# Kernel optimization log

Measured on AMD Instinct MI355X. Metric: run time of the kernel, lower is better.

The kernel has to match this reference:

```python
import jax, jax.numpy as jnp
import numpy as np

KER = 8

def _gelu(x):
    return jax.nn.gelu(x, approximate=False)

def _conv3x3(x, w, b):
    y = jax.lax.conv_general_dilated(x, w, (1, 1), 'SAME',
                                     dimension_numbers=('NCHW', 'OIHW', 'NCHW'))
    return y + b[None, :, None, None]

def _unfold(x):
    # F.unfold(kernel=8, stride=8): [B,C,H,W] -> [B, C*64, L], C-major then kh,kw
    B, C, H, W = x.shape
    Hb, Wb = H // KER, W // KER
    p = x.reshape(B, C, Hb, KER, Wb, KER).transpose(0, 1, 3, 5, 2, 4)
    return p.reshape(B, C * KER * KER, Hb * Wb)

def _fold(cols, H, W):
    # inverse of _unfold (non-overlapping patches)
    B, CK, L = cols.shape
    C = CK // (KER * KER)
    Hb, Wb = H // KER, W // KER
    p = cols.reshape(B, C, KER, KER, Hb, Wb).transpose(0, 1, 4, 2, 5, 3)
    return p.reshape(B, C, H, W)

def _bn(x, g, b, eps=1e-5):
    # train-mode BatchNorm1d on [B, C, L]: stats over (B, L) per channel
    m = x.mean(axis=(0, 2), keepdims=True)
    v = x.var(axis=(0, 2), keepdims=True)
    return (x - m) * jax.lax.rsqrt(v + eps) * g[None, :, None] + b[None, :, None]


def setup_inputs() -> dict:
    key = jax.random.key(0)
    ks = jax.random.split(key, 10)
    ind, d, hid = 64, 1024, 256
    f = lambda k, s: jax.random.normal(k, s, dtype=jnp.float32) * 0.02
    return {
        'feat': jax.random.normal(ks[0], (4, ind, 256, 256), dtype=jnp.float32),
        'w_enc': f(ks[1], (ind, ind, 3, 3)), 'b_enc': jnp.zeros((ind,), jnp.float32),
        'w_k': f(ks[2], (ind, ind, 3, 3)), 'b_k': jnp.zeros((ind,), jnp.float32),
        'w_v': f(ks[3], (ind, ind, 3, 3)), 'b_v': jnp.zeros((ind,), jnp.float32),
        'fcq_w': f(ks[4], (d, ind * KER * KER)), 'fcq_b': jnp.zeros((d,), jnp.float32),
        'fck_w': f(ks[5], (d, ind * KER * KER)), 'fck_b': jnp.zeros((d,), jnp.float32),
        'bnq_g': jnp.ones((d,), jnp.float32), 'bnq_b': jnp.zeros((d,), jnp.float32),
        'bnk_g': jnp.ones((d,), jnp.float32), 'bnk_b': jnp.zeros((d,), jnp.float32),
        'ff1_w': f(ks[6], (hid, ind)), 'ff1_b': jnp.zeros((hid,), jnp.float32),
        'ff2_w': f(ks[7], (ind, hid)), 'ff2_b': jnp.zeros((ind,), jnp.float32),
    }


def reference(feat, w_enc, b_enc, w_k, b_k, w_v, b_v,
              fcq_w, fcq_b, fck_w, fck_b, bnq_g, bnq_b, bnk_g, bnk_b,
              ff1_w, ff1_b, ff2_w, ff2_b):
    B, C, H, W = feat.shape
    fk = _gelu(_conv3x3(feat, w_k, b_k))
    fv = _gelu(_conv3x3(feat, w_v, b_v))
    refer = _gelu(_conv3x3(feat, w_enc, b_enc))
    q_un = _unfold(refer).transpose(0, 2, 1)   # [B, L, C*64]
    k_un = _unfold(fk).transpose(0, 2, 1)
    v_un = _unfold(fv).transpose(0, 2, 1)
    q = jnp.einsum('blc,dc->bld', q_un, fcq_w) + fcq_b
    q = _bn(q.transpose(0, 2, 1), bnq_g, bnq_b).transpose(0, 2, 1)  # [B, L, 1024]
    k = jnp.einsum('blc,dc->bld', k_un, fck_w) + fck_b
    k = _bn(k.transpose(0, 2, 1), bnk_g, bnk_b).transpose(0, 2, 1)
    scores = jnp.einsum('bld,bmd->blm', q, k) / jnp.sqrt(jnp.float32(q.shape[2]))
    attn = jax.nn.softmax(scores, axis=2)
    out = jnp.einsum('blm,bmc->blc', attn, v_un).transpose(0, 2, 1)  # [B, C*64, L]
    out = _fold(out, H, W)
    h = _gelu(jnp.einsum('bchw,oc->bohw', out, ff1_w) + ff1_b[None, :, None, None])
    h = _gelu(jnp.einsum('bchw,oc->bohw', h, ff2_w) + ff2_b[None, :, None, None])
    return h + feat
```

## Files before the change

kernel.cpp:

```cpp
#include <hip/hip_runtime.h>

typedef unsigned short u16;
typedef float f4 __attribute__((ext_vector_type(4)));
typedef float f32x4 __attribute__((ext_vector_type(4)));
typedef short bf16x8 __attribute__((ext_vector_type(8)));
typedef u16 u16x8 __attribute__((ext_vector_type(8)));
typedef u16 u16x4 __attribute__((ext_vector_type(4)));

__device__ __forceinline__ u16 f2bf(float f){
  unsigned u = __float_as_uint(f);
  u = (u + 0x7FFFu + ((u>>16)&1u)) >> 16;
  return (u16)u;
}
__device__ __forceinline__ float bf2f(u16 u){
  return __uint_as_float(((unsigned)u)<<16);
}
__device__ __forceinline__ float gelu_f(float x){
  float y = 1.5957691216057308f*(x + 0.044715f*x*x*x);
  y = fminf(y, 30.0f);
  float t = __expf(y);
  float r = __builtin_amdgcn_rcpf(t + 1.0f);
  return 0.5f*x*(1.0f + (t - 1.0f)*r);
}

typedef __attribute__((address_space(1))) const unsigned int as1_cuint;
typedef __attribute__((address_space(3))) unsigned int as3_uint;
__device__ __forceinline__ void gload_lds16(const void* g, void* l){
  __builtin_amdgcn_global_load_lds((as1_cuint*)g, (as3_uint*)l, 16, 0, 0);
}

__global__ __launch_bounds__(256) void to_nhwc(
    const float* __restrict__ F, u16* __restrict__ O)
{
  __shared__ float tile[64][65];
  const int t = threadIdx.x, b = blockIdx.y;
  const long px0 = (long)blockIdx.x*64;
  const float* Fb = F + (long)b*64*65536;
  #pragma unroll
  for (int i = 0; i < 4; ++i){
    const int ch = (t>>4) + i*16;
    const int pxo = (t&15)*4;
    f4 v = *(const f4*)&Fb[(long)ch*65536 + px0 + pxo];
    tile[ch][pxo]=v[0]; tile[ch][pxo+1]=v[1]; tile[ch][pxo+2]=v[2]; tile[ch][pxo+3]=v[3];
  }
  __syncthreads();
  const int px = t & 63, ch0 = (t>>6)*16;
  u16x8 o0, o1;
  #pragma unroll
  for (int j = 0; j < 8; ++j){ o0[j]=f2bf(tile[ch0+j][px]); o1[j]=f2bf(tile[ch0+8+j][px]); }
  u16* Ob = O + ((long)b*65536 + px0 + px)*64 + ch0;
  *(u16x8*)Ob = o0; *(u16x8*)(Ob+8) = o1;
}

__global__ __launch_bounds__(256) void wt_prep(
    const float* __restrict__ we, const float* __restrict__ wk,
    const float* __restrict__ wv, u16* __restrict__ Wt2)
{
  const int i = blockIdx.x*256 + threadIdx.x;
  const int cio = i & 31;
  const int t1 = i >> 5;
  const int n  = t1 % 192;
  const int t2 = t1 / 192;
  const int kc = t2 & 1, p = t2 >> 1;
  const int dy = p/3, dx = p - dy*3;
  const int ci = kc*32 + cio;
  const float* W = (n < 64) ? we : (n < 128) ? wk : wv;
  const int co = n & 63;
  Wt2[i] = f2bf(W[((co*64 + ci)*3 + dy)*3 + dx]);
}

__global__ __launch_bounds__(512,2) void conv_mfma(
    const u16* __restrict__ X, const u16* __restrict__ Wt2,
    const float* __restrict__ be, const float* __restrict__ bk, const float* __restrict__ bv,
    u16* __restrict__ Aq, u16* __restrict__ Ak, u16* __restrict__ Vl)
{
  __shared__ __align__(16) u16 smem[24576];
  const int t = threadIdx.x, lane = t & 63, wvi = t >> 6;
  const int bx = blockIdx.x, by = blockIdx.y, b = blockIdx.z;
  const int x0 = bx*16, y0 = by*8;
  const u16* Xb = X + (long)b*4194304;

  #pragma unroll
  for (int j = 0; j < 3; ++j){
    const int id = t + j*512;
    if (id < 1440){
      const int row = id / 144, rem = id - row*144, col = rem >> 3, ck = rem & 7;
      const int y = y0 - 1 + row, x = x0 - 1 + col;
      int4 v = {0,0,0,0};
      if ((unsigned)y < 256u && (unsigned)x < 256u)
        v = *(const int4*)(Xb + ((long)y*256 + x)*64 + ck*8);
      *(int4*)&smem[((row*18 + col)*8 + (ck ^ (col&7)))*8] = v;
    }
  }
  __syncthreads();

  const int wm4 = (wvi>>2)*4;
  const int wn  = (wvi&3)*48;
  const int fr = lane & 15, fo = lane >> 4;
  f32x4 acc[4][3] = {};

  #pragma unroll
  for (int dy = 0; dy < 3; ++dy)
  #pragma unroll
  for (int dx = 0; dx < 3; ++dx){
    const int p = dy*3 + dx;
    #pragma unroll
    for (int kc = 0; kc < 2; ++kc){
      bf16x8 af[4], bfv[3];
      const u16* wp = Wt2 + ((long)(p*2 + kc)*192 + wn + fr)*32 + fo*8;
      #pragma unroll
      for (int ni = 0; ni < 3; ++ni)
        bfv[ni] = *(const bf16x8*)(wp + ni*16*32);
      #pragma unroll
      for (int mi = 0; mi < 4; ++mi){
        const int row = wm4 + mi + dy;
        const int col = fr + dx;
        af[mi] = *(const bf16x8*)&smem[((row*18 + col)*8 + ((kc*4+fo) ^ (col&7)))*8];
      }
      #pragma unroll
      for (int mi = 0; mi < 4; ++mi)
        #pragma unroll
        for (int ni = 0; ni < 3; ++ni)
          acc[mi][ni] = __builtin_amdgcn_mfma_f32_16x16x32_bf16(af[mi], bfv[ni], acc[mi][ni], 0, 0, 0);
    }
  }
  __syncthreads();

  const int c0 = fo*4;
  const int lloc = c0 >> 3, kw0 = c0 & 7;
  #pragma unroll
  for (int ni = 0; ni < 3; ++ni){
    const int n = wn + ni*16 + fr;
    const int mat = n >> 6, co = n & 63;
    const float bias = (mat==0) ? be[co] : (mat==1) ? bk[co] : bv[co];
    #pragma unroll
    for (int mi = 0; mi < 4; ++mi){
      const int r = wm4 + mi;
      u16x4 o;
      #pragma unroll
      for (int rg = 0; rg < 4; ++rg) o[rg] = f2bf(gelu_f(acc[mi][ni][rg] + bias));
      const int e = ((mat*2 + lloc)*64 + co)*64 + ((r*8 + kw0) ^ ((co&7)<<3));
      *(u16x4*)&smem[e] = o;
    }
  }
  __syncthreads();

  const int l_lo = by*32 + bx*2;
  const int co_r = t >> 3, sw = (t&7) ^ (co_r&7);
  const int eoff = co_r*64 + sw*8;
  #pragma unroll
  for (int i = 0; i < 6; ++i){
    const int mat = i >> 1, ll = i & 1;
    u16x8 v = *(const u16x8*)&smem[(mat*2 + ll)*4096 + eoff];
    u16* dst = (mat==0 ? Aq : mat==1 ? Ak : Vl)
             + ((long)b*1024 + l_lo + ll)*4096 + t*8;
    *(u16x8*)dst = v;
  }
}

__global__ __launch_bounds__(256) void v_tr(
    const u16* __restrict__ S, u16* __restrict__ D)
{
  __shared__ u16 tl[64][72];
  const int t = threadIdx.x, b = blockIdx.z;
  const int ck0 = blockIdx.x*64, l0 = blockIdx.y*64;
  const u16* Sb = S + (long)b*4194304;
  u16* Db = D + (long)b*4194304;
  #pragma unroll
  for (int j = 0; j < 2; ++j){
    const int li = (t>>3) + j*32, cko = (t&7)*8;
    *(u16x8*)&tl[li][cko] = *(const u16x8*)(Sb + (long)(l0+li)*4096 + ck0 + cko);
  }
  __syncthreads();
  #pragma unroll
  for (int j = 0; j < 2; ++j){
    const int cki = (t>>3) + j*32, lo = (t&7)*8;
    u16x8 v;
    #pragma unroll
    for (int e = 0; e < 8; ++e) v[e] = tl[lo+e][cki];
    *(u16x8*)(Db + (long)(ck0+cki)*1024 + l0 + lo) = v;
  }
}

template<int EPI>
__global__ __launch_bounds__(256,3) void gemm_bt(
    const u16* __restrict__ A, long sA,
    const u16* __restrict__ B, long sB, const int zshB,
    void* __restrict__ Cv, long sC,
    const int M, const int N, const int K,
    float* __restrict__ bnstats)
{
  const int bI = blockIdx.z;
  const u16* Ab = A + (long)bI*sA;
  const u16* Bb = B + (long)(bI>>zshB)*sB;
  const int m0 = blockIdx.x*128, n0 = blockIdx.y*128;
  __shared__ __align__(16) u16 As[8192];
  __shared__ __align__(16) u16 Bs[8192];
  const int t = threadIdx.x, lane = t & 63, wv = t >> 6;
  const int wm = (wv>>1)*64, wn = (wv&1)*64;
  const int fr = lane & 15, fo = lane >> 4;
  f32x4 acc[4][4] = {};
  const int c0 = wv*128 + lane, c1 = c0 + 64;
  const u16* Ag0 = Ab + (long)(m0 + (c0>>2))*K + (c0&3)*8;
  const u16* Ag1 = Ab + (long)(m0 + (c1>>2))*K + (c1&3)*8;
  const u16* Bg0 = Bb + (long)(n0 + (c0>>2))*K + (c0&3)*8;
  const u16* Bg1 = Bb + (long)(n0 + (c1>>2))*K + (c1&3)*8;
  const int lo0 = wv*1024;
  gload_lds16(Ag0, &As[lo0]);
  gload_lds16(Ag1, &As[lo0 + 512]);
  gload_lds16(Bg0, &Bs[lo0]);
  gload_lds16(Bg1, &Bs[lo0 + 512]);
  const int nk = K >> 5;
  int cur = 0;
  for (int ki = 0; ki < nk; ++ki){
    __syncthreads();
    if (ki + 1 < nk){
      const int k0 = (ki + 1) << 5;
      const int so = ((cur^1) << 12) + lo0;
      gload_lds16(Ag0 + k0, &As[so]);
      gload_lds16(Ag1 + k0, &As[so + 512]);
      gload_lds16(Bg0 + k0, &Bs[so]);
      gload_lds16(Bg1 + k0, &Bs[so + 512]);
    }
    const int ro = cur << 12;
    bf16x8 af[4], bfv[4];
    #pragma unroll
    for (int i = 0; i < 4; ++i){
      af[i]  = *(const bf16x8*)&As[ro + (wm + i*16 + fr)*32 + fo*8];
      bfv[i] = *(const bf16x8*)&Bs[ro + (wn + i*16 + fr)*32 + fo*8];
    }
    #pragma unroll
    for (int mi = 0; mi < 4; ++mi)
      #pragma unroll
      for (int ni = 0; ni < 4; ++ni)
        acc[mi][ni] = __builtin_amdgcn_mfma_f32_16x16x32_bf16(af[mi], bfv[ni], acc[mi][ni], 0, 0, 0);
    cur ^= 1;
  }
  if (EPI == 0){
    float* Cf = (float*)Cv + (long)bI*sC;
    #pragma unroll
    for (int mi = 0; mi < 4; ++mi)
      #pragma unroll
      for (int ni = 0; ni < 4; ++ni){
        const int col = n0 + wn + ni*16 + fr;
        #pragma unroll
        for (int r = 0; r < 4; ++r){
          const int row = m0 + wm + mi*16 + fo*4 + r;
          Cf[(long)row*N + col] = acc[mi][ni][r];
        }
      }
  } else if (EPI == 1) {
    u16* O = (u16*)Cv;
    #pragma unroll
    for (int mi = 0; mi < 4; ++mi)
      #pragma unroll
      for (int ni = 0; ni < 4; ++ni){
        const int col = n0 + wn + ni*16 + fr;
        const int c = col >> 6, khh = (col>>3)&7, kww = col&7;
        #pragma unroll
        for (int r = 0; r < 4; ++r){
          const int row = m0 + wm + mi*16 + fo*4 + r;
          const int hb = row >> 5, wbb = row & 31;
          O[(((long)bI*65536 + (hb*8+khh)*256 + wbb*8 + kww)<<6) + c] = f2bf(acc[mi][ni][r]);
        }
      }
  } else {
    u16* Cb = (u16*)Cv + (long)bI*sC;
    #pragma unroll
    for (int mi = 0; mi < 4; ++mi)
      #pragma unroll
      for (int ni = 0; ni < 4; ++ni){
        const int col = n0 + wn + ni*16 + fr;
        const int row0 = m0 + wm + mi*16 + fo*4;
        u16x4 o;
        #pragma unroll
        for (int r = 0; r < 4; ++r) o[r] = f2bf(acc[mi][ni][r]);
        *(u16x4*)&Cb[(long)col*M + row0] = o;
      }
    const int sel = bI >> 2;
    float* sums = bnstats + sel*2048;
    #pragma unroll
    for (int ni = 0; ni < 4; ++ni){
      float s = 0.f, q = 0.f;
      #pragma unroll
      for (int mi = 0; mi < 4; ++mi)
        #pragma unroll
        for (int r = 0; r < 4; ++r){
          const float v = acc[mi][ni][r];
          s += v; q += v*v;
        }
      s += __shfl_xor(s, 16); s += __shfl_xor(s, 32);
      q += __shfl_xor(q, 16); q += __shfl_xor(q, 32);
      if (fo == 0){
        const int col = n0 + wn + ni*16 + fr;
        atomicAdd(&sums[col], s);
        atomicAdd(&sums[1024 + col], q);
      }
    }
  }
}

__global__ __launch_bounds__(256,3) void ff1_mfma(
    const u16* __restrict__ X, const u16* __restrict__ W1b,
    const float* __restrict__ B1, u16* __restrict__ H1)
{
  const int t = threadIdx.x, lane = t & 63, wv = t >> 6;
  const long m0 = (long)blockIdx.x*128 + (wv>>1)*64;
  const int n0 = blockIdx.y*128 + (wv&1)*64;
  const int fr = lane & 15, fo = lane >> 4;
  f32x4 acc[4][4] = {};
  #pragma unroll
  for (int k0 = 0; k0 < 64; k0 += 32){
    bf16x8 af[4], bfv[4];
    #pragma unroll
    for (int i = 0; i < 4; ++i){
      af[i]  = *(const bf16x8*)(X   + (m0 + i*16 + fr)*64 + k0 + fo*8);
      bfv[i] = *(const bf16x8*)(W1b + (long)(n0 + i*16 + fr)*64 + k0 + fo*8);
    }
    #pragma unroll
    for (int mi = 0; mi < 4; ++mi)
      #pragma unroll
      for (int ni = 0; ni < 4; ++ni)
        acc[mi][ni] = __builtin_amdgcn_mfma_f32_16x16x32_bf16(af[mi], bfv[ni], acc[mi][ni], 0, 0, 0);
  }
  #pragma unroll
  for (int ni = 0; ni < 4; ++ni){
    const int col = n0 + ni*16 + fr;
    const float bc = B1[col];
    #pragma unroll
    for (int mi = 0; mi < 4; ++mi){
      const long row = m0 + mi*16 + fo*4;
      #pragma unroll
      for (int r = 0; r < 4; ++r)
        H1[(row + r)*256 + col] = f2bf(gelu_f(acc[mi][ni][r] + bc));
    }
  }
}

__global__ __launch_bounds__(256,3) void ff2_mfma(
    const u16* __restrict__ H1, const u16* __restrict__ W2b,
    const float* __restrict__ B2, const float* __restrict__ F,
    float* __restrict__ OUT)
{
  const int t = threadIdx.x, lane = t & 63, wv = t >> 6;
  const long m0 = (long)blockIdx.x*256 + wv*64;
  const int fr = lane & 15, fo = lane >> 4;
  f32x4 acc[4][4] = {};
  for (int k0 = 0; k0 < 256; k0 += 32){
    bf16x8 af[4], bfv[4];
    #pragma unroll
    for (int i = 0; i < 4; ++i){
      af[i]  = *(const bf16x8*)(H1  + (m0 + i*16 + fr)*256 + k0 + fo*8);
      bfv[i] = *(const bf16x8*)(W2b + (long)(i*16 + fr)*256 + k0 + fo*8);
    }
    #pragma unroll
    for (int mi = 0; mi < 4; ++mi)
      #pragma unroll
      for (int ni = 0; ni < 4; ++ni)
        acc[mi][ni] = __builtin_amdgcn_mfma_f32_16x16x32_bf16(af[mi], bfv[ni], acc[mi][ni], 0, 0, 0);
  }
  #pragma unroll
  for (int ni = 0; ni < 4; ++ni){
    const int c = ni*16 + fr;
    const float bc = B2[c];
    #pragma unroll
    for (int mi = 0; mi < 4; ++mi){
      const long p = m0 + mi*16 + fo*4;
      const int b = (int)(p >> 16), pp = (int)(p & 65535);
      const long idx = ((long)(b*64 + c))*65536 + pp;
      const f4 fres = *(const f4*)&F[idx];
      f4 o;
      #pragma unroll
      for (int r = 0; r < 4; ++r) o[r] = gelu_f(acc[mi][ni][r] + bc) + fres[r];
      *(f4*)&OUT[idx] = o;
    }
  }
}

__global__ __launch_bounds__(256) void cvt_w(
    const float* __restrict__ Wq, const float* __restrict__ Wk,
    u16* __restrict__ Oq, u16* __restrict__ Ok)
{
  const long i = ((long)blockIdx.x*256 + threadIdx.x)*4;
  const float* s = blockIdx.y ? Wk : Wq;
  u16* d = blockIdx.y ? Ok : Oq;
  f4 v = *(const f4*)&s[i];
  u16x4 o; o[0]=f2bf(v[0]); o[1]=f2bf(v[1]); o[2]=f2bf(v[2]); o[3]=f2bf(v[3]);
  *(u16x4*)&d[i] = o;
}

__global__ __launch_bounds__(256) void cvt_ffw(
    const float* __restrict__ W1, const float* __restrict__ W2,
    u16* __restrict__ O1, u16* __restrict__ O2)
{
  const long i = ((long)blockIdx.x*256 + threadIdx.x)*4;
  const float* s = blockIdx.y ? W2 : W1;
  u16* d = blockIdx.y ? O2 : O1;
  f4 v = *(const f4*)&s[i];
  u16x4 o; o[0]=f2bf(v[0]); o[1]=f2bf(v[1]); o[2]=f2bf(v[2]); o[3]=f2bf(v[3]);
  *(u16x4*)&d[i] = o;
}

__global__ void bn_fin2(float* __restrict__ stats,
                        const float* __restrict__ gq, const float* __restrict__ bq,
                        const float* __restrict__ gk, const float* __restrict__ bk)
{
  const int sel = blockIdx.y;
  const int d = blockIdx.x*256 + threadIdx.x;
  if (d >= 1024) return;
  const float* sum   = stats + sel*2048;
  const float* sumsq = sum + 1024;
  const float* g    = sel ? gk : gq;
  const float* beta = sel ? bk : bq;
  const float m  = sum[d]   * (1.f/4096.f);
  const float vv = sumsq[d] * (1.f/4096.f) - m*m;
  const float sc = g[d] * rsqrtf(vv + 1e-5f);
  stats[4096 + sel*2048 + d]        = sc;
  stats[4096 + sel*2048 + 1024 + d] = beta[d] - m*sc;
}

__global__ __launch_bounds__(256) void bn_apply_t(
    const u16* __restrict__ QT, const float* __restrict__ stats,
    u16* __restrict__ Y)
{
  __shared__ u16 tl[64][72];
  const int t = threadIdx.x, zi = blockIdx.z;
  const int d0 = blockIdx.x*64, l0 = blockIdx.y*64;
  const int sel = zi >> 2;
  const u16* S = QT + (long)zi*1048576;
  u16* D = Y + (long)zi*1048576;
  const float* scp = stats + 4096 + sel*2048;
  const float* shp = scp + 1024;
  #pragma unroll
  for (int j = 0; j < 2; ++j){
    const int di = (t>>3) + j*32, lo = (t&7)*8;
    const int d = d0 + di;
    const float sc = scp[d], sh = shp[d];
    u16x8 v = *(const u16x8*)(S + (long)d*1024 + l0 + lo);
    u16x8 o;
    #pragma unroll
    for (int e = 0; e < 8; ++e) o[e] = f2bf(bf2f(v[e])*sc + sh);
    *(u16x8*)&tl[di][lo] = o;
  }
  __syncthreads();
  #pragma unroll
  for (int j = 0; j < 2; ++j){
    const int li = (t>>3) + j*32, dof = (t&7)*8;
    u16x8 v;
    #pragma unroll
    for (int e = 0; e < 8; ++e) v[e] = tl[dof+e][li];
    *(u16x8*)(D + (long)(l0+li)*1024 + d0 + dof) = v;
  }
}

__global__ __launch_bounds__(256) void softmax_k(
    const float* __restrict__ S, u16* __restrict__ P)
{
  const long row = blockIdx.x;
  const float* p = S + row*1024;
  const int t = threadIdx.x;
  f4 v = *(const f4*)&p[t*4];
  v *= 0.03125f;
  float mx = fmaxf(fmaxf(v[0],v[1]), fmaxf(v[2],v[3]));
  #pragma unroll
  for (int o = 1; o < 64; o <<= 1) mx = fmaxf(mx, __shfl_xor(mx, o));
  __shared__ float red[4], red2[4];
  if ((t & 63) == 0) red[t>>6] = mx;
  __syncthreads();
  mx = fmaxf(fmaxf(red[0],red[1]), fmaxf(red[2],red[3]));
  f4 e;
  e[0]=__expf(v[0]-mx); e[1]=__expf(v[1]-mx); e[2]=__expf(v[2]-mx); e[3]=__expf(v[3]-mx);
  float sm = e[0]+e[1]+e[2]+e[3];
  #pragma unroll
  for (int o = 1; o < 64; o <<= 1) sm += __shfl_xor(sm, o);
  if ((t & 63) == 0) red2[t>>6] = sm;
  __syncthreads();
  sm = red2[0]+red2[1]+red2[2]+red2[3];
  const float inv = 1.0f/sm;
  u16x4 o4; o4[0]=f2bf(e[0]*inv); o4[1]=f2bf(e[1]*inv); o4[2]=f2bf(e[2]*inv); o4[3]=f2bf(e[3]*inv);
  *(u16x4*)&P[row*1024 + t*4] = o4;
}

extern "C" void kernel_launch(void* const* d_in, const int* in_sizes, int n_in,
                              void* d_out, int out_size, void* d_ws, size_t ws_size,
                              hipStream_t stream)
{
  const float* feat  = (const float*)d_in[0];
  const float* w_enc = (const float*)d_in[1];
  const float* b_enc = (const float*)d_in[2];
  const float* w_k   = (const float*)d_in[3];
  const float* b_k   = (const float*)d_in[4];
  const float* w_v   = (const float*)d_in[5];
  const float* b_v   = (const float*)d_in[6];
  const float* fcq_w = (const float*)d_in[7];
  const float* fck_w = (const float*)d_in[9];
  const float* bnq_g = (const float*)d_in[11];
  const float* bnq_b = (const float*)d_in[12];
  const float* bnk_g = (const float*)d_in[13];
  const float* bnk_b = (const float*)d_in[14];
  const float* ff1w  = (const float*)d_in[15];
  const float* ff1b  = (const float*)d_in[16];
  const float* ff2w  = (const float*)d_in[17];
  const float* ff2b  = (const float*)d_in[18];

  char* ws = (char*)d_ws;
  u16*   Aq      = (u16*)  (ws);
  u16*   Ak      = (u16*)  (ws + (32ull<<20));
  u16*   Vc      = (u16*)  (ws + (64ull<<20));
  u16*   Wq      = (u16*)  (ws + (96ull<<20));
  u16*   Wk      = (u16*)  (ws + (104ull<<20));
  u16*   q_bf    = (u16*)  (ws + (112ull<<20));
  u16*   k_bf    = (u16*)  (ws + (120ull<<20));
  u16*   qk_rawT = (u16*)  (ws + (128ull<<20));
  float* scores  = (float*)(ws + (160ull<<20));
  u16*   attn    = (u16*)  (ws + (176ull<<20));
  u16*   out_nhwc= (u16*)  (ws + (184ull<<20));
  u16*   NX      = (u16*)  (ws + (128ull<<20));
  u16*   Vl      = (u16*)  (ws + (160ull<<20));
  u16*   Wt2     = (u16*)  (ws + (216ull<<20));
  float* stats   = (float*)(ws + (217ull<<20));
  u16*   W1b     = (u16*)  (ws + (218ull<<20));
  u16*   W2b     = (u16*)  (ws + (218ull<<20) + 65536);
  u16*   h1      = (u16*)  (ws);

  hipMemsetAsync(stats, 0, 4096*sizeof(float), stream);

  to_nhwc<<<dim3(1024,4), 256, 0, stream>>>(feat, NX);
  wt_prep<<<dim3(432), 256, 0, stream>>>(w_enc, w_k, w_v, Wt2);
  conv_mfma<<<dim3(16,32,4), 512, 0, stream>>>(NX, Wt2, b_enc, b_k, b_v, Aq, Ak, Vl);
  v_tr<<<dim3(64,16,4), 256, 0, stream>>>(Vl, Vc);
  cvt_w<<<dim3(4096,2), 256, 0, stream>>>(fcq_w, fck_w, Wq, Wk);
  cvt_ffw<<<dim3(16,2), 256, 0, stream>>>(ff1w, ff2w, W1b, W2b);

  gemm_bt<2><<<dim3(8,8,8),  256, 0, stream>>>(Aq, 4194304, Wq, 4194304, 2,
                                               qk_rawT, 1048576, 1024, 1024, 4096, stats);

  bn_fin2<<<dim3(4,2), 256, 0, stream>>>(stats, bnq_g, bnq_b, bnk_g, bnk_b);
  bn_apply_t<<<dim3(16,16,8), 256, 0, stream>>>(qk_rawT, stats, q_bf);

  gemm_bt<0><<<dim3(8,8,4),  256, 0, stream>>>(q_bf, 1048576, k_bf, 1048576, 0,
                                               scores, 1048576, 1024, 1024, 1024, nullptr);
  softmax_k<<<dim3(4096), 256, 0, stream>>>(scores, attn);

  gemm_bt<1><<<dim3(8,32,4), 256, 0, stream>>>(attn, 1048576, Vc, 4194304, 0,
                                               out_nhwc, 0, 1024, 4096, 1024, nullptr);

  ff1_mfma<<<dim3(2048,2), 256, 0, stream>>>(out_nhwc, W1b, ff1b, h1);
  ff2_mfma<<<dim3(1024), 256, 0, stream>>>(h1, W2b, ff2b, feat, (float*)d_out);
}
```

Measured before the change: 537.8 us.

## Deepen GEMM K-step to 64, add XCD-aware block remap and MFMA priority

The batched bf16 GEMM now stages two 32-wide K halves per iteration, doubling LDS buffers so each barrier covers twice as many MFMAs. Block indices are remapped so consecutive blocks dispatched to the same XCD share A/B tiles in that XCD's L2. s_setprio raises wave priority around the MFMA bursts. The larger LDS footprint lowers launch bounds occupancy from 3 to 2 blocks per CU, which may reduce latency hiding.

```diff
diff --git a/kernel.cpp b/kernel.cpp
--- a/kernel.cpp
+++ b/kernel.cpp
@@ -182,20 +182,31 @@
   }
 }
 
+__device__ __forceinline__ void xcd_map(int gxl, int gyl, int n8l,
+                                        int& bx, int& by, int& bz){
+  const int s = blockIdx.x + (blockIdx.y<<gxl) + (blockIdx.z<<(gxl+gyl));
+  const int orig = ((s & 7) << n8l) + (s >> 3);
+  bx = orig & ((1<<gxl)-1);
+  by = (orig >> gxl) & ((1<<gyl)-1);
+  bz = orig >> (gxl+gyl);
+}
+
 template<int EPI>
-__global__ __launch_bounds__(256,3) void gemm_bt(
+__global__ __launch_bounds__(256,2) void gemm_bt128(
     const u16* __restrict__ A, long sA,
     const u16* __restrict__ B, long sB, const int zshB,
     void* __restrict__ Cv, long sC,
     const int M, const int N, const int K,
-    float* __restrict__ bnstats)
-{
-  const int bI = blockIdx.z;
+    float* __restrict__ bnstats,
+    const int gxl, const int gyl, const int n8l)
+{
+  int bx, by, bI;
+  xcd_map(gxl, gyl, n8l, bx, by, bI);
   const u16* Ab = A + (long)bI*sA;
   const u16* Bb = B + (long)(bI>>zshB)*sB;
-  const int m0 = blockIdx.x*128, n0 = blockIdx.y*128;
-  __shared__ __align__(16) u16 As[8192];
-  __shared__ __align__(16) u16 Bs[8192];
+  const int m0 = bx*128, n0 = by*128;
+  __shared__ __align__(16) u16 As[16384];
+  __shared__ __align__(16) u16 Bs[16384];
   const int t = threadIdx.x, lane = t & 63, wv = t >> 6;
   const int wm = (wv>>1)*64, wn = (wv&1)*64;
   const int fr = lane & 15, fo = lane >> 4;
@@ -205,37 +216,45 @@
   const u16* Ag1 = Ab + (long)(m0 + (c1>>2))*K + (c1&3)*8;
   const u16* Bg0 = Bb + (long)(n0 + (c0>>2))*K + (c0&3)*8;
   const u16* Bg1 = Bb + (long)(n0 + (c1>>2))*K + (c1&3)*8;
-  const int lo0 = wv*1024;
-  gload_lds16(Ag0, &As[lo0]);
-  gload_lds16(Ag1, &As[lo0 + 512]);
-  gload_lds16(Bg0, &Bs[lo0]);
-  gload_lds16(Bg1, &Bs[lo0 + 512]);
-  const int nk = K >> 5;
+#define STAGEH(slot, h, kofs) { \
+    u16* a_ = &As[(((slot)*2+(h))<<12) + wv*1024]; \
+    u16* b_ = &Bs[(((slot)*2+(h))<<12) + wv*1024]; \
+    const int ko_ = (kofs) + 32*(h); \
+    gload_lds16(Ag0 + ko_, a_); \
+    gload_lds16(Ag1 + ko_, a_ + 512); \
+    gload_lds16(Bg0 + ko_, b_); \
+    gload_lds16(Bg1 + ko_, b_ + 512); }
+  STAGEH(0, 0, 0)
+  STAGEH(0, 1, 0)
+  const int nk = K >> 6;
   int cur = 0;
   for (int ki = 0; ki < nk; ++ki){
     __syncthreads();
     if (ki + 1 < nk){
-      const int k0 = (ki + 1) << 5;
-      const int so = ((cur^1) << 12) + lo0;
-      gload_lds16(Ag0 + k0, &As[so]);
-      gload_lds16(Ag1 + k0, &As[so + 512]);
-      gload_lds16(Bg0 + k0, &Bs[so]);
-      gload_lds16(Bg1 + k0, &Bs[so + 512]);
-    }
-    const int ro = cur << 12;
-    bf16x8 af[4], bfv[4];
-    #pragma unroll
-    for (int i = 0; i < 4; ++i){
-      af[i]  = *(const bf16x8*)&As[ro + (wm + i*16 + fr)*32 + fo*8];
-      bfv[i] = *(const bf16x8*)&Bs[ro + (wn + i*16 + fr)*32 + fo*8];
-    }
-    #pragma unroll
-    for (int mi = 0; mi < 4; ++mi)
-      #pragma unroll
-      for (int ni = 0; ni < 4; ++ni)
-        acc[mi][ni] = __builtin_amdgcn_mfma_f32_16x16x32_bf16(af[mi], bfv[ni], acc[mi][ni], 0, 0, 0);
+      const int k0 = (ki + 1) << 6;
+      STAGEH(cur^1, 0, k0)
+      STAGEH(cur^1, 1, k0)
+    }
+    #pragma unroll
+    for (int h = 0; h < 2; ++h){
+      const int ro = ((cur*2 + h) << 12);
+      bf16x8 af[4], bfv[4];
+      #pragma unroll
+      for (int i = 0; i < 4; ++i){
+        af[i]  = *(const bf16x8*)&As[ro + (wm + i*16 + fr)*32 + fo*8];
+        bfv[i] = *(const bf16x8*)&Bs[ro + (wn + i*16 + fr)*32 + fo*8];
+      }
+      __builtin_amdgcn_s_setprio(1);
+      #pragma unroll
+      for (int mi = 0; mi < 4; ++mi)
+        #pragma unroll
+        for (int ni = 0; ni < 4; ++ni)
+          acc[mi][ni] = __builtin_amdgcn_mfma_f32_16x16x32_bf16(af[mi], bfv[ni], acc[mi][ni], 0, 0, 0);
+      __builtin_amdgcn_s_setprio(0);
+    }
     cur ^= 1;
   }
+#undef STAGEH
   if (EPI == 0){
     float* Cf = (float*)Cv + (long)bI*sC;
     #pragma unroll
@@ -532,18 +551,21 @@
   cvt_w<<<dim3(4096,2), 256, 0, stream>>>(fcq_w, fck_w, Wq, Wk);
   cvt_ffw<<<dim3(16,2), 256, 0, stream>>>(ff1w, ff2w, W1b, W2b);
 
-  gemm_bt<2><<<dim3(8,8,8),  256, 0, stream>>>(Aq, 4194304, Wq, 4194304, 2,
-                                               qk_rawT, 1048576, 1024, 1024, 4096, stats);
+  gemm_bt128<2><<<dim3(8,8,8), 256, 0, stream>>>(Aq, 4194304, Wq, 4194304, 2,
+                                                 qk_rawT, 1048576, 1024, 1024, 4096, stats,
+                                                 3, 3, 6);
 
   bn_fin2<<<dim3(4,2), 256, 0, stream>>>(stats, bnq_g, bnq_b, bnk_g, bnk_b);
   bn_apply_t<<<dim3(16,16,8), 256, 0, stream>>>(qk_rawT, stats, q_bf);
 
-  gemm_bt<0><<<dim3(8,8,4),  256, 0, stream>>>(q_bf, 1048576, k_bf, 1048576, 0,
-                                               scores, 1048576, 1024, 1024, 1024, nullptr);
+  gemm_bt128<0><<<dim3(8,8,4), 256, 0, stream>>>(q_bf, 1048576, k_bf, 1048576, 0,
+                                                 scores, 1048576, 1024, 1024, 1024, nullptr,
+                                                 3, 3, 5);
   softmax_k<<<dim3(4096), 256, 0, stream>>>(scores, attn);
 
-  gemm_bt<1><<<dim3(8,32,4), 256, 0, stream>>>(attn, 1048576, Vc, 4194304, 0,
-                                               out_nhwc, 0, 1024, 4096, 1024, nullptr);
+  gemm_bt128<1><<<dim3(8,32,4), 256, 0, stream>>>(attn, 1048576, Vc, 4194304, 0,
+                                                  out_nhwc, 0, 1024, 4096, 1024, nullptr,
+                                                  3, 5, 7);
 
   ff1_mfma<<<dim3(2048,2), 256, 0, stream>>>(out_nhwc, W1b, ff1b, h1);
   ff2_mfma<<<dim3(1024), 256, 0, stream>>>(h1, W2b, ff2b, feat, (float*)d_out);
```

Measured after the change: 523.2 us. 1.03x faster.
